# Performance work log

Hardware: AMD Instinct MI355X
Metric: run time of the kernel (lower is better)

The kernel has to match this reference:

```python
import jax, jax.numpy as jnp
import numpy as np

DIM = 192
HEADS = 8
EPS = 1e-12  # torch F.normalize eps


def setup_inputs() -> dict:
    key = jax.random.key(0)
    k1, k2, k3, k4 = jax.random.split(key, 4)
    b, c, h, w = 2, DIM, 256, 256
    x = jax.random.normal(k1, (b, c, h, w), dtype=jnp.float32)
    # 1x1 conv weights stored as (out, in)
    qkv_w = jax.random.normal(k2, (3 * c, c), dtype=jnp.float32) * (1.0 / np.sqrt(c))
    # depthwise 3x3, groups = 3c -> OIHW with I=1
    dw_w = jax.random.normal(k3, (3 * c, 1, 3, 3), dtype=jnp.float32) * (1.0 / 3.0)
    proj_w = jax.random.normal(k4, (c, c), dtype=jnp.float32) * (1.0 / np.sqrt(c))
    temperature = jnp.ones((HEADS, 1, 1), dtype=jnp.float32)
    return {"x": x, "qkv_w": qkv_w, "dw_w": dw_w, "proj_w": proj_w,
            "temperature": temperature}


def _l2norm(t):
    n = jnp.sqrt(jnp.sum(t * t, axis=-1, keepdims=True))
    return t / jnp.maximum(n, EPS)


def reference(x, qkv_w, dw_w, proj_w, temperature):
    b, c, h, w = x.shape
    # 1x1 conv (pointwise) -> depthwise 3x3 conv
    qkv = jnp.einsum('oc,bchw->bohw', qkv_w, x)  # (b, 3c, h, w)
    qkv = jax.lax.conv_general_dilated(
        qkv, dw_w, window_strides=(1, 1), padding='SAME',
        feature_group_count=3 * c,
        dimension_numbers=('NCHW', 'OIHW', 'NCHW'))
    q, k, v = jnp.split(qkv, 3, axis=1)
    # faithful reshape: full C channels per head, spatial dim split by heads
    q = q.reshape(b, HEADS, c, -1)
    k = k.reshape(b, HEADS, c, -1)
    v = v.reshape(b, HEADS, c, -1)
    q = _l2norm(q)
    k = _l2norm(k)
    attn = jnp.einsum('bhcn,bhdn->bhcd', q, k) * temperature  # (b,H,c,c)
    attn = jax.nn.softmax(attn, axis=-1)
    out = jnp.einsum('bhcd,bhdn->bhcn', attn, v)
    out = out.reshape(b, c, h, w)
    out = jnp.einsum('oc,bchw->bohw', proj_w, out)
    return out
```

## Files before the change

### kernel.cpp

```cpp
#include <hip/hip_runtime.h>
#include <math.h>

typedef unsigned short u16;
typedef unsigned int   u32;
typedef short bf16x8 __attribute__((ext_vector_type(8)));
typedef float f32x4  __attribute__((ext_vector_type(4)));

#define MFMA16(a,b,c) __builtin_amdgcn_mfma_f32_16x16x32_bf16((a),(b),(c),0,0,0)

__device__ __forceinline__ float bf2f(u16 h){ u32 u=((u32)h)<<16; return __uint_as_float(u); }
__device__ __forceinline__ u16 f2bf(float f){ u32 u=__float_as_uint(f); return (u16)((u+0x7fffu+((u>>16)&1u))>>16); }

__device__ __forceinline__ void stc(u16* p, float v){ *p = f2bf(v); }
__device__ __forceinline__ void stc(float* p, float v){ *p = v; }
__device__ __forceinline__ void ld4(const float* p, float* v){ float4 x=*(const float4*)p; v[0]=x.x;v[1]=x.y;v[2]=x.z;v[3]=x.w; }
__device__ __forceinline__ void ld4(const u16* p, float* v){ ushort4 x=*(const ushort4*)p; v[0]=bf2f(x.x);v[1]=bf2f(x.y);v[2]=bf2f(x.z);v[3]=bf2f(x.w); }

__global__ void cvt_kernel(const float* __restrict__ in, u16* __restrict__ out, int n){
  int i = blockIdx.x*256 + threadIdx.x;
  if (i < n) out[i] = f2bf(in[i]);
}

template<typename TIN>
__global__ __launch_bounds__(256) void transpose_kernel(
    const TIN* __restrict__ in, u16* __restrict__ out,
    long in_hi, long in_lo, long out_slab, int in_pitch)
{
  __shared__ float tile[64][65];
  const int t = threadIdx.x;
  const int z = blockIdx.z;
  const TIN* ip = in + (long)(z>>3)*in_hi + (long)(z&7)*in_lo;
  u16* op = out + (long)z*out_slab;
  const int s0 = blockIdx.x*64, c0 = blockIdx.y*64;
  const int rl = t>>4, cc = (t&15)*4;
#pragma unroll
  for (int rr=0; rr<4; rr++){
    int row = rr*16 + rl;
    float v[4];
    ld4(ip + (long)(c0+row)*in_pitch + s0 + cc, v);
    tile[row][cc+0]=v[0]; tile[row][cc+1]=v[1]; tile[row][cc+2]=v[2]; tile[row][cc+3]=v[3];
  }
  __syncthreads();
#pragma unroll
  for (int wr=0; wr<4; wr++){
    int sl = wr*16 + rl;
    ushort4 s;
    s.x = f2bf(tile[cc+0][sl]); s.y = f2bf(tile[cc+1][sl]);
    s.z = f2bf(tile[cc+2][sl]); s.w = f2bf(tile[cc+3][sl]);
    *(ushort4*)(op + (long)(s0+sl)*192 + c0 + cc) = s;
  }
}

template<typename TC>
__global__ __launch_bounds__(256) void gemm_nt_kernel(
    const u16* __restrict__ A, const u16* __restrict__ B, TC* __restrict__ C,
    int M, long sB, long sC)
{
  __shared__ __align__(16) u16 As[128*32];
  __shared__ __align__(16) u16 Bs[128*32];
  const int t = threadIdx.x, w = t>>6, l = t&63;
  const int mt = blockIdx.x, nt = blockIdx.y, bz = blockIdx.z;
  const int m0 = mt*128, n0 = nt*128;
  const u16* Bb = B + (long)bz*sB + (long)n0*192;
  const int rq = t>>2, qq = (t&3)*8;
  int ar0 = m0 + rq;      if (ar0 >= M) ar0 = M-1;
  int ar1 = m0 + 64 + rq; if (ar1 >= M) ar1 = M-1;
  f32x4 acc[4][4];
#pragma unroll
  for (int i=0;i<4;i++)
#pragma unroll
    for (int j=0;j<4;j++) acc[i][j] = f32x4{0.f,0.f,0.f,0.f};

  for (int k0=0; k0<192; k0+=32){
    uint4 va0 = *(const uint4*)(A + (long)ar0*192 + k0 + qq);
    uint4 va1 = *(const uint4*)(A + (long)ar1*192 + k0 + qq);
    uint4 vb0 = *(const uint4*)(Bb + (long)rq*192 + k0 + qq);
    uint4 vb1 = *(const uint4*)(Bb + (long)(64+rq)*192 + k0 + qq);
    __syncthreads();
    *(uint4*)(As + t*8) = va0;
    *(uint4*)(As + (256+t)*8) = va1;
    *(uint4*)(Bs + t*8) = vb0;
    *(uint4*)(Bs + (256+t)*8) = vb1;
    __syncthreads();
    const u16* ap = As + ((w>>1)*64 + (l&15))*32 + (l>>4)*8;
    const u16* bp = Bs + ((w&1)*64 + (l&15))*32 + (l>>4)*8;
    bf16x8 a[4], b[4];
#pragma unroll
    for (int i=0;i<4;i++){ a[i] = *(const bf16x8*)(ap + i*512); b[i] = *(const bf16x8*)(bp + i*512); }
#pragma unroll
    for (int i=0;i<4;i++)
#pragma unroll
      for (int j=0;j<4;j++) acc[i][j] = MFMA16(a[i], b[j], acc[i][j]);
  }
  const int mw = m0 + (w>>1)*64, nw = n0 + (w&1)*64;
  TC* Cb = C + (long)bz*sC;
#pragma unroll
  for (int i=0;i<4;i++){
#pragma unroll
    for (int r=0;r<4;r++){
      int row = mw + i*16 + (l>>4)*4 + r;
      if (row < M){
        TC* cp = Cb + (long)row*65536 + nw + (l&15);
#pragma unroll
        for (int j=0;j<4;j++) stc(cp + j*16, acc[i][j][r]);
      }
    }
  }
}

__global__ __launch_bounds__(256) void dwconv_kernel(
    const u16* __restrict__ in, const float* __restrict__ w9s,
    u16* __restrict__ out, float* __restrict__ norms)
{
  const int bo = blockIdx.x >> 4;
  const int rt = blockIdx.x & 15;
  const int o  = bo % 576;
  const u16* ip = in + (long)bo*65536L;
  u16* op = out + (long)bo*65536L;
  float w[9];
#pragma unroll
  for (int i=0;i<9;i++) w[i] = w9s[o*9+i];
  __shared__ float tile[18*256];
  const int t = threadIdx.x;
  for (int vi=t; vi<1152; vi+=256){
    int row = vi>>6, col = (vi&63)<<2;
    int g = rt*16 - 1 + row;
    if (g >= 0 && g < 256){
      ushort4 u = *(const ushort4*)(ip + g*256 + col);
      tile[row*256+col+0]=bf2f(u.x); tile[row*256+col+1]=bf2f(u.y);
      tile[row*256+col+2]=bf2f(u.z); tile[row*256+col+3]=bf2f(u.w);
    } else {
      tile[row*256+col+0]=0.f; tile[row*256+col+1]=0.f;
      tile[row*256+col+2]=0.f; tile[row*256+col+3]=0.f;
    }
  }
  __syncthreads();
  const int col = t;
  const bool cl = (col>0), cr = (col<255);
  float ss = 0.f;
#pragma unroll 4
  for (int ro=0; ro<16; ro++){
    const float* r0 = &tile[(ro+0)*256+col];
    const float* r1 = &tile[(ro+1)*256+col];
    const float* r2 = &tile[(ro+2)*256+col];
    float acc = r0[0]*w[1] + r1[0]*w[4] + r2[0]*w[7];
    if (cl) acc += r0[-1]*w[0] + r1[-1]*w[3] + r2[-1]*w[6];
    if (cr) acc += r0[1]*w[2] + r1[1]*w[5] + r2[1]*w[8];
    op[(rt*16+ro)*256 + col] = f2bf(acc);
    ss += acc*acc;
  }
#pragma unroll
  for (int off=32; off>=1; off>>=1) ss += __shfl_xor(ss, off);
  __shared__ float red[4];
  if ((t&63)==0) red[t>>6] = ss;
  __syncthreads();
  if (t==0 && o < 384){
    atomicAdd(&norms[bo*8 + (rt>>1)], red[0]+red[1]+red[2]+red[3]);
  }
}

__global__ __launch_bounds__(256) void gemm_qk_kernel(
    const u16* __restrict__ conv, float* __restrict__ part)
{
  __shared__ __align__(16) u16 As[64*64];
  __shared__ __align__(16) u16 Bs[64*64];
  const int t = threadIdx.x, w = t>>6, l = t&63;
  const int mt = blockIdx.x, nt = blockIdx.y, z = blockIdx.z;
  const int bh = z>>3, sl = z&7;
  const int b = bh>>3, h = bh&7;
  const u16* Q  = conv + (long)b*37748736L + (long)h*1572864L;
  const u16* Kp = Q + 12582912L;
  const int m0 = mt*64, n0 = nt*64;
  const int rq = t>>3, qq = (t&7)*8;
  const long qo0 = (long)(m0+rq)*8192 + qq;
  const long qo1 = (long)(m0+32+rq)*8192 + qq;
  const long ko0 = (long)(n0+rq)*8192 + qq;
  const long ko1 = (long)(n0+32+rq)*8192 + qq;
  f32x4 acc[2][2];
#pragma unroll
  for (int i=0;i<2;i++)
#pragma unroll
    for (int j=0;j<2;j++) acc[i][j] = f32x4{0.f,0.f,0.f,0.f};
  const int kbeg = sl*1024;
  for (int k0=kbeg; k0<kbeg+1024; k0+=64){
    uint4 vq0 = *(const uint4*)(Q  + qo0 + k0);
    uint4 vq1 = *(const uint4*)(Q  + qo1 + k0);
    uint4 vk0 = *(const uint4*)(Kp + ko0 + k0);
    uint4 vk1 = *(const uint4*)(Kp + ko1 + k0);
    __syncthreads();
    *(uint4*)(As + t*8) = vq0;
    *(uint4*)(As + (256+t)*8) = vq1;
    *(uint4*)(Bs + t*8) = vk0;
    *(uint4*)(Bs + (256+t)*8) = vk1;
    __syncthreads();
    const u16* ap = As + ((w>>1)*32 + (l&15))*64 + (l>>4)*8;
    const u16* bp = Bs + ((w&1)*32 + (l&15))*64 + (l>>4)*8;
#pragma unroll
    for (int ks=0; ks<2; ks++){
      bf16x8 a0 = *(const bf16x8*)(ap + ks*32);
      bf16x8 a1 = *(const bf16x8*)(ap + 1024 + ks*32);
      bf16x8 b0 = *(const bf16x8*)(bp + ks*32);
      bf16x8 b1 = *(const bf16x8*)(bp + 1024 + ks*32);
      acc[0][0]=MFMA16(a0,b0,acc[0][0]); acc[0][1]=MFMA16(a0,b1,acc[0][1]);
      acc[1][0]=MFMA16(a1,b0,acc[1][0]); acc[1][1]=MFMA16(a1,b1,acc[1][1]);
    }
  }
  float* P = part + (long)z*36864L;
  const int mw = m0 + (w>>1)*32, nw = n0 + (w&1)*32;
#pragma unroll
  for (int i=0;i<2;i++)
#pragma unroll
    for (int j=0;j<2;j++)
#pragma unroll
      for (int r=0;r<4;r++)
        P[(long)(mw + i*16 + (l>>4)*4 + r)*192 + nw + j*16 + (l&15)] = acc[i][j][r];
}

__global__ __launch_bounds__(64) void softmax_kernel(
    const float* __restrict__ part, const float* __restrict__ temp,
    const float* __restrict__ norms, u16* __restrict__ attn)
{
  const int rg = blockIdx.x;
  const int bh = rg/192, r = rg - bh*192;
  const int b = bh>>3, h = bh&7;
  const int t = threadIdx.x;
  const float tp = temp[h];
  const float sq = norms[(b*576 + 24*h + (r>>3))*8 + (r&7)];
  const float invq = 1.f/fmaxf(sqrtf(sq), 1e-12f);
  const float* P = part + (long)bh*8L*36864L + (long)r*192;
  float lv[3];
#pragma unroll
  for (int j=0;j<3;j++){
    int col = t + j*64;
    float s = 0.f;
#pragma unroll
    for (int ks=0; ks<8; ks++) s += P[(long)ks*36864L + col];
    float sk = norms[(b*576 + 192 + 24*h + (col>>3))*8 + (col&7)];
    float invk = 1.f/fmaxf(sqrtf(sk), 1e-12f);
    lv[j] = s*invq*invk*tp;
  }
  float mx = fmaxf(lv[0], fmaxf(lv[1], lv[2]));
#pragma unroll
  for (int o=32;o>=1;o>>=1) mx = fmaxf(mx, __shfl_xor(mx, o));
  float e[3], sum = 0.f;
#pragma unroll
  for (int j=0;j<3;j++){ e[j] = expf(lv[j]-mx); sum += e[j]; }
#pragma unroll
  for (int o=32;o>=1;o>>=1) sum += __shfl_xor(sum, o);
  const float inv = 1.f/sum;
  u16* ap = attn + (long)bh*36864L + (long)r*192;
#pragma unroll
  for (int j=0;j<3;j++) ap[t + j*64] = f2bf(e[j]*inv);
}

__global__ __launch_bounds__(256) void gemm_av_kernel(
    const u16* __restrict__ VT, const u16* __restrict__ attn, u16* __restrict__ out_sc)
{
  __shared__ __align__(16) char smem[69632];
  u16* As = (u16*)smem;
  u16* Bs = (u16*)(smem + 8192);
  const int t = threadIdx.x, w = t>>6, l = t&63;
  const int mt = blockIdx.x, nt = blockIdx.y, bh = blockIdx.z;
  const int b = bh>>3, h = bh&7;
  const u16* Av = VT + (long)bh*1572864L;
  const u16* Bt = attn + (long)bh*36864L;
  const int m0 = mt*128, n0 = nt*128;
  const int rq = t>>2, qq = (t&3)*8;
  int br0 = n0 + rq;      if (br0 > 191) br0 = 191;
  int br1 = n0 + 64 + rq; if (br1 > 191) br1 = 191;
  f32x4 acc[4][4];
#pragma unroll
  for (int i=0;i<4;i++)
#pragma unroll
    for (int j=0;j<4;j++) acc[i][j] = f32x4{0.f,0.f,0.f,0.f};
  for (int k0=0; k0<192; k0+=32){
    uint4 va0 = *(const uint4*)(Av + (long)(m0+rq)*192 + k0 + qq);
    uint4 va1 = *(const uint4*)(Av + (long)(m0+64+rq)*192 + k0 + qq);
    uint4 vb0 = *(const uint4*)(Bt + (long)br0*192 + k0 + qq);
    uint4 vb1 = *(const uint4*)(Bt + (long)br1*192 + k0 + qq);
    __syncthreads();
    *(uint4*)(As + t*8) = va0;
    *(uint4*)(As + (256+t)*8) = va1;
    *(uint4*)(Bs + t*8) = vb0;
    *(uint4*)(Bs + (256+t)*8) = vb1;
    __syncthreads();
    const u16* ap = As + ((w>>1)*64 + (l&15))*32 + (l>>4)*8;
    const u16* bp = Bs + ((w&1)*64 + (l&15))*32 + (l>>4)*8;
    bf16x8 a[4], bb[4];
#pragma unroll
    for (int i=0;i<4;i++){ a[i] = *(const bf16x8*)(ap + i*512); bb[i] = *(const bf16x8*)(bp + i*512); }
#pragma unroll
    for (int i=0;i<4;i++)
#pragma unroll
      for (int j=0;j<4;j++) acc[i][j] = MFMA16(a[i], bb[j], acc[i][j]);
  }
  __syncthreads();
  float* wb = (float*)smem + w*4352;
#pragma unroll
  for (int i=0;i<4;i++)
#pragma unroll
    for (int j=0;j<4;j++)
#pragma unroll
      for (int r=0;r<4;r++)
        wb[(i*16 + (l>>4)*4 + r)*68 + j*16 + (l&15)] = acc[i][j][r];
  __syncthreads();
  const int c0w = nt*128 + (w&1)*64;
  if (c0w < 192){
    const int cb = 24*h + (c0w>>3);
    const int mw = m0 + (w>>1)*64;
    u16* ob = out_sc + (long)b*12582912L + cb;
    const int nl0 = l>>3, sb = l&7;
#pragma unroll
    for (int ri=0; ri<8; ri++){
      int nl = ri*8 + nl0;
      const float* src = wb + nl*68 + sb;
      u32 d0 = (u32)f2bf(src[0])  | ((u32)f2bf(src[8])  << 16);
      u32 d1 = (u32)f2bf(src[16]) | ((u32)f2bf(src[24]) << 16);
      u32 d2 = (u32)f2bf(src[32]) | ((u32)f2bf(src[40]) << 16);
      u32 d3 = (u32)f2bf(src[48]) | ((u32)f2bf(src[56]) << 16);
      *(uint4*)(ob + ((long)sb*8192 + mw + nl)*192) = make_uint4(d0,d1,d2,d3);
    }
  }
}

extern "C" void kernel_launch(void* const* d_in, const int* in_sizes, int n_in,
                              void* d_out, int out_size, void* d_ws, size_t ws_size,
                              hipStream_t stream)
{
  const float* x      = (const float*)d_in[0];
  const float* qkv_w  = (const float*)d_in[1];
  const float* dw_w   = (const float*)d_in[2];
  const float* proj_w = (const float*)d_in[3];
  const float* temp   = (const float*)d_in[4];
  float* out = (float*)d_out;

  char* ws = (char*)d_ws;
  u16*   xT      = (u16*)(ws + 0);
  u16*   conv    = (u16*)(ws + 0);
  u16*   qkv_raw = (u16*)(ws + 150994944);
  u16*   VT      = (u16*)(ws + 150994944);
  u16*   out_sc  = (u16*)(ws + 201326592);
  float* part    = (float*)(ws + 251658240);
  u16*   attn    = (u16*)(ws + 270532608);
  u16*   wq_bf   = (u16*)(ws + 301989888);
  u16*   wp_bf   = (u16*)(ws + 302211072);
  float* norms   = (float*)(ws + 302284800);

  hipMemsetAsync(norms, 0, 9216*sizeof(float), stream);

  cvt_kernel<<<dim3(432), 256, 0, stream>>>(qkv_w, wq_bf, 110592);
  cvt_kernel<<<dim3(144), 256, 0, stream>>>(proj_w, wp_bf, 36864);

  transpose_kernel<float><<<dim3(1024, 3, 2), 256, 0, stream>>>(
      x, xT, 0L, 12582912L, 12582912L, 65536);

  gemm_nt_kernel<u16><<<dim3(5, 512, 2), 256, 0, stream>>>(
      wq_bf, xT, qkv_raw, 576, 12582912L, 37748736L);

  dwconv_kernel<<<dim3(1152*16), 256, 0, stream>>>(qkv_raw, dw_w, conv, norms);

  transpose_kernel<u16><<<dim3(128, 3, 16), 256, 0, stream>>>(
      conv + 25165824L, VT, 37748736L, 1572864L, 1572864L, 8192);

  gemm_qk_kernel<<<dim3(3, 3, 128), 256, 0, stream>>>(conv, part);

  softmax_kernel<<<dim3(3072), 64, 0, stream>>>(part, temp, norms, attn);

  gemm_av_kernel<<<dim3(64, 2, 16), 256, 0, stream>>>(VT, attn, out_sc);

  gemm_nt_kernel<float><<<dim3(2, 512, 2), 256, 0, stream>>>(
      wp_bf, out_sc, out, 192, 12582912L, 12582912L);
}
```

Baseline: 457.7 us.

## Use direct global-to-LDS loads in GEMMs, register-tile dwconv, fuse prep kernels

The three MFMA GEMM kernels now fill their shared-memory tiles with global_load_lds, which copies 16 bytes per lane straight into LDS and skips the round trip through VGPRs. The depthwise conv is reworked so each thread computes a 4x4 output block from float4 LDS reads, using a padded tile with zeroed halo columns, and writes packed ushort4 stores. The two weight-conversion kernels and the memset of the norms buffer are merged into one prep kernel to cut launch count. The direct-to-LDS path depends on the per-lane LDS layout matching what the builtin writes, and the new dwconv raises register use per thread.

```diff
diff --git a/kernel.cpp b/kernel.cpp
--- a/kernel.cpp
+++ b/kernel.cpp
@@ -11,14 +11,21 @@
 __device__ __forceinline__ float bf2f(u16 h){ u32 u=((u32)h)<<16; return __uint_as_float(u); }
 __device__ __forceinline__ u16 f2bf(float f){ u32 u=__float_as_uint(f); return (u16)((u+0x7fffu+((u>>16)&1u))>>16); }
 
+__device__ __forceinline__ void gl2lds(const u16* g, u16* l){
+  __builtin_amdgcn_global_load_lds((const __attribute__((address_space(1))) u32*)g,
+                                   (__attribute__((address_space(3))) u32*)l, 16, 0, 0);
+}
 __device__ __forceinline__ void stc(u16* p, float v){ *p = f2bf(v); }
 __device__ __forceinline__ void stc(float* p, float v){ *p = v; }
 __device__ __forceinline__ void ld4(const float* p, float* v){ float4 x=*(const float4*)p; v[0]=x.x;v[1]=x.y;v[2]=x.z;v[3]=x.w; }
 __device__ __forceinline__ void ld4(const u16* p, float* v){ ushort4 x=*(const ushort4*)p; v[0]=bf2f(x.x);v[1]=bf2f(x.y);v[2]=bf2f(x.z);v[3]=bf2f(x.w); }
 
-__global__ void cvt_kernel(const float* __restrict__ in, u16* __restrict__ out, int n){
+__global__ void prep_kernel(const float* __restrict__ qkv_w, const float* __restrict__ proj_w,
+                            u16* __restrict__ wq, u16* __restrict__ wp, float* __restrict__ norms){
   int i = blockIdx.x*256 + threadIdx.x;
-  if (i < n) out[i] = f2bf(in[i]);
+  if (i < 110592) wq[i] = f2bf(qkv_w[i]);
+  else if (i < 147456) wp[i-110592] = f2bf(proj_w[i-110592]);
+  else if (i < 156672) norms[i-147456] = 0.f;
 }
 
 template<typename TIN>
@@ -72,15 +79,11 @@
     for (int j=0;j<4;j++) acc[i][j] = f32x4{0.f,0.f,0.f,0.f};
 
   for (int k0=0; k0<192; k0+=32){
-    uint4 va0 = *(const uint4*)(A + (long)ar0*192 + k0 + qq);
-    uint4 va1 = *(const uint4*)(A + (long)ar1*192 + k0 + qq);
-    uint4 vb0 = *(const uint4*)(Bb + (long)rq*192 + k0 + qq);
-    uint4 vb1 = *(const uint4*)(Bb + (long)(64+rq)*192 + k0 + qq);
-    __syncthreads();
-    *(uint4*)(As + t*8) = va0;
-    *(uint4*)(As + (256+t)*8) = va1;
-    *(uint4*)(Bs + t*8) = vb0;
-    *(uint4*)(Bs + (256+t)*8) = vb1;
+    __syncthreads();
+    gl2lds(A + (long)ar0*192 + k0 + qq, As + t*8);
+    gl2lds(A + (long)ar1*192 + k0 + qq, As + (256+t)*8);
+    gl2lds(Bb + (long)rq*192 + k0 + qq, Bs + t*8);
+    gl2lds(Bb + (long)(64+rq)*192 + k0 + qq, Bs + (256+t)*8);
     __syncthreads();
     const u16* ap = As + ((w>>1)*64 + (l&15))*32 + (l>>4)*8;
     const u16* bp = Bs + ((w&1)*64 + (l&15))*32 + (l>>4)*8;
@@ -120,34 +123,57 @@
   float w[9];
 #pragma unroll
   for (int i=0;i<9;i++) w[i] = w9s[o*9+i];
-  __shared__ float tile[18*256];
+  __shared__ float tile[18*264];
   const int t = threadIdx.x;
+  if (t < 144){
+    int row = t >> 3, c = t & 7;
+    tile[row*264 + ((c<4) ? c : 256+c)] = 0.f;
+  }
   for (int vi=t; vi<1152; vi+=256){
     int row = vi>>6, col = (vi&63)<<2;
     int g = rt*16 - 1 + row;
+    float4 f;
     if (g >= 0 && g < 256){
       ushort4 u = *(const ushort4*)(ip + g*256 + col);
-      tile[row*256+col+0]=bf2f(u.x); tile[row*256+col+1]=bf2f(u.y);
-      tile[row*256+col+2]=bf2f(u.z); tile[row*256+col+3]=bf2f(u.w);
-    } else {
-      tile[row*256+col+0]=0.f; tile[row*256+col+1]=0.f;
-      tile[row*256+col+2]=0.f; tile[row*256+col+3]=0.f;
+      f = make_float4(bf2f(u.x), bf2f(u.y), bf2f(u.z), bf2f(u.w));
+    } else f = make_float4(0.f,0.f,0.f,0.f);
+    *(float4*)&tile[row*264 + 4 + col] = f;
+  }
+  __syncthreads();
+  const int tx = t & 63, ty = t >> 6;
+  const float* base = &tile[4 + tx*4];
+  float acc[4][4];
+#pragma unroll
+  for (int i=0;i<4;i++)
+#pragma unroll
+    for (int j=0;j<4;j++) acc[i][j] = 0.f;
+#pragma unroll
+  for (int r=0; r<6; r++){
+    const float* row = base + (ty*4 + r)*264;
+    float4 L = *(const float4*)(row - 4);
+    float4 M = *(const float4*)(row);
+    float4 R = *(const float4*)(row + 4);
+    const float lf=L.w, m0=M.x, m1=M.y, m2=M.z, m3=M.w, rg=R.x;
+#pragma unroll
+    for (int ro=0; ro<4; ro++){
+      if (r-ro >= 0 && r-ro <= 2){
+        const int wr = (r-ro)*3;
+        acc[ro][0] = fmaf(w[wr],lf, fmaf(w[wr+1],m0, fmaf(w[wr+2],m1, acc[ro][0])));
+        acc[ro][1] = fmaf(w[wr],m0, fmaf(w[wr+1],m1, fmaf(w[wr+2],m2, acc[ro][1])));
+        acc[ro][2] = fmaf(w[wr],m1, fmaf(w[wr+1],m2, fmaf(w[wr+2],m3, acc[ro][2])));
+        acc[ro][3] = fmaf(w[wr],m2, fmaf(w[wr+1],m3, fmaf(w[wr+2],rg, acc[ro][3])));
+      }
     }
   }
-  __syncthreads();
-  const int col = t;
-  const bool cl = (col>0), cr = (col<255);
   float ss = 0.f;
-#pragma unroll 4
-  for (int ro=0; ro<16; ro++){
-    const float* r0 = &tile[(ro+0)*256+col];
-    const float* r1 = &tile[(ro+1)*256+col];
-    const float* r2 = &tile[(ro+2)*256+col];
-    float acc = r0[0]*w[1] + r1[0]*w[4] + r2[0]*w[7];
-    if (cl) acc += r0[-1]*w[0] + r1[-1]*w[3] + r2[-1]*w[6];
-    if (cr) acc += r0[1]*w[2] + r1[1]*w[5] + r2[1]*w[8];
-    op[(rt*16+ro)*256 + col] = f2bf(acc);
-    ss += acc*acc;
+#pragma unroll
+  for (int ro=0; ro<4; ro++){
+    ushort4 s;
+    s.x = f2bf(acc[ro][0]); s.y = f2bf(acc[ro][1]);
+    s.z = f2bf(acc[ro][2]); s.w = f2bf(acc[ro][3]);
+    *(ushort4*)(op + (rt*16 + ty*4 + ro)*256 + tx*4) = s;
+#pragma unroll
+    for (int j=0;j<4;j++) ss = fmaf(acc[ro][j], acc[ro][j], ss);
   }
 #pragma unroll
   for (int off=32; off>=1; off>>=1) ss += __shfl_xor(ss, off);
@@ -183,15 +209,11 @@
     for (int j=0;j<2;j++) acc[i][j] = f32x4{0.f,0.f,0.f,0.f};
   const int kbeg = sl*1024;
   for (int k0=kbeg; k0<kbeg+1024; k0+=64){
-    uint4 vq0 = *(const uint4*)(Q  + qo0 + k0);
-    uint4 vq1 = *(const uint4*)(Q  + qo1 + k0);
-    uint4 vk0 = *(const uint4*)(Kp + ko0 + k0);
-    uint4 vk1 = *(const uint4*)(Kp + ko1 + k0);
-    __syncthreads();
-    *(uint4*)(As + t*8) = vq0;
-    *(uint4*)(As + (256+t)*8) = vq1;
-    *(uint4*)(Bs + t*8) = vk0;
-    *(uint4*)(Bs + (256+t)*8) = vk1;
+    __syncthreads();
+    gl2lds(Q  + qo0 + k0, As + t*8);
+    gl2lds(Q  + qo1 + k0, As + (256+t)*8);
+    gl2lds(Kp + ko0 + k0, Bs + t*8);
+    gl2lds(Kp + ko1 + k0, Bs + (256+t)*8);
     __syncthreads();
     const u16* ap = As + ((w>>1)*32 + (l&15))*64 + (l>>4)*8;
     const u16* bp = Bs + ((w&1)*32 + (l&15))*64 + (l>>4)*8;
@@ -274,15 +296,11 @@
 #pragma unroll
     for (int j=0;j<4;j++) acc[i][j] = f32x4{0.f,0.f,0.f,0.f};
   for (int k0=0; k0<192; k0+=32){
-    uint4 va0 = *(const uint4*)(Av + (long)(m0+rq)*192 + k0 + qq);
-    uint4 va1 = *(const uint4*)(Av + (long)(m0+64+rq)*192 + k0 + qq);
-    uint4 vb0 = *(const uint4*)(Bt + (long)br0*192 + k0 + qq);
-    uint4 vb1 = *(const uint4*)(Bt + (long)br1*192 + k0 + qq);
-    __syncthreads();
-    *(uint4*)(As + t*8) = va0;
-    *(uint4*)(As + (256+t)*8) = va1;
-    *(uint4*)(Bs + t*8) = vb0;
-    *(uint4*)(Bs + (256+t)*8) = vb1;
+    __syncthreads();
+    gl2lds(Av + (long)(m0+rq)*192 + k0 + qq, As + t*8);
+    gl2lds(Av + (long)(m0+64+rq)*192 + k0 + qq, As + (256+t)*8);
+    gl2lds(Bt + (long)br0*192 + k0 + qq, Bs + t*8);
+    gl2lds(Bt + (long)br1*192 + k0 + qq, Bs + (256+t)*8);
     __syncthreads();
     const u16* ap = As + ((w>>1)*64 + (l&15))*32 + (l>>4)*8;
     const u16* bp = Bs + ((w&1)*64 + (l&15))*32 + (l>>4)*8;
@@ -346,10 +364,7 @@
   u16*   wp_bf   = (u16*)(ws + 302211072);
   float* norms   = (float*)(ws + 302284800);
 
-  hipMemsetAsync(norms, 0, 9216*sizeof(float), stream);
-
-  cvt_kernel<<<dim3(432), 256, 0, stream>>>(qkv_w, wq_bf, 110592);
-  cvt_kernel<<<dim3(144), 256, 0, stream>>>(proj_w, wp_bf, 36864);
+  prep_kernel<<<dim3(612), 256, 0, stream>>>(qkv_w, proj_w, wq_bf, wp_bf, norms);
 
   transpose_kernel<float><<<dim3(1024, 3, 2), 256, 0, stream>>>(
       x, xT, 0L, 12582912L, 12582912L, 65536);
```

Measured after the change: 452.9 us. About the same (-1.1%).
